# Performance work log

Measured on AMD Instinct MI355X. Metric: run time of the kernel, lower is better.

The kernel has to match this reference:

```python
import jax, jax.numpy as jnp
import numpy as np

N = 50000      # nodes
E = 800000     # edges (avg degree 16)
D = 128        # d_model
C = 2          # num_classes
F_IN = 8       # GCNConv(8, d_model)


def setup_inputs() -> dict:
    key = jax.random.key(0)
    ks = jax.random.split(key, 12)
    s = 0.05  # weight init scale
    return {
        "feature_vec": jax.random.normal(ks[0], (N, F_IN), dtype=jnp.float32),
        "bboxes": jax.random.uniform(ks[1], (N, 4), dtype=jnp.float32),
        "bbox_indices": jnp.arange(N, dtype=jnp.int64) if jax.config.jax_enable_x64 else jnp.arange(N, dtype=jnp.int32),
        "edge_index": jax.random.randint(ks[2], (2, E), 0, N, dtype=jnp.int32),
        "W1": jax.random.normal(ks[3], (F_IN, D), dtype=jnp.float32) * s,
        "b1": jnp.zeros((D,), dtype=jnp.float32),
        "W2": jax.random.normal(ks[4], (D, D), dtype=jnp.float32) * s,
        "b2": jnp.zeros((D,), dtype=jnp.float32),
        "lin1_W": jax.random.normal(ks[5], (2 * D, D), dtype=jnp.float32) * s,
        "lin1_b": jnp.zeros((D,), dtype=jnp.float32),
        "linf_W": jax.random.normal(ks[6], (D, C), dtype=jnp.float32) * s,
        "linf_b": jnp.zeros((C,), dtype=jnp.float32),
    }


def gcn_conv(x, W, b, edge_index, n):
    """PyG GCNConv: add self-loops, symmetric D^-1/2 A D^-1/2 normalization."""
    x = x @ W                                   # [n, out]
    sl = jnp.arange(n, dtype=edge_index.dtype)
    row = jnp.concatenate([edge_index[0], sl])  # source
    col = jnp.concatenate([edge_index[1], sl])  # target
    ones = jnp.ones(row.shape[0], dtype=x.dtype)
    deg = jax.ops.segment_sum(ones, col, num_segments=n)  # >= 1 due to self-loops
    dinv = jax.lax.rsqrt(deg)
    norm = dinv[row] * dinv[col]                # [E + n]
    msg = x[row] * norm[:, None]                # gather + scale
    out = jax.ops.segment_sum(msg, col, num_segments=n)   # scatter-aggregate
    return out + b


def reference(feature_vec, bboxes, bbox_indices, edge_index,
              W1, b1, W2, b2, lin1_W, lin1_b, linf_W, linf_b):
    n = feature_vec.shape[0]
    x = jax.nn.relu(gcn_conv(feature_vec, W1, b1, edge_index, n))
    x = jax.nn.relu(gcn_conv(x, W2, b2, edge_index, n))
    x1 = x[edge_index[0]]                        # [E, D]
    x2 = x[edge_index[1]]                        # [E, D]
    xpair = jnp.concatenate([x1, x2], axis=-1)   # [E, 2D]
    xpair = jax.nn.relu(xpair @ lin1_W + lin1_b)
    xfin = xpair @ linf_W + linf_b               # [E, C]
    probs = jax.nn.log_softmax(xfin, axis=-1)
    bbox_pairs = jnp.concatenate([bboxes[edge_index[0]], bboxes[edge_index[1]]], axis=-1)  # [E, 8]
    bbox_index_pairs = jnp.stack([bbox_indices[edge_index[0]], bbox_indices[edge_index[1]]], axis=1)  # [E, 2]
    return (probs, bbox_pairs, bbox_index_pairs)
```

## Files before the change

kernel.cpp:

```cpp
#include <hip/hip_runtime.h>
#include <hip/hip_bf16.h>
#include <math.h>


typedef __attribute__((ext_vector_type(8))) short short8;
typedef __attribute__((ext_vector_type(4))) float f32x4;
typedef __attribute__((ext_vector_type(2))) float fv2;

__device__ inline ushort f2bf(float f) {
    union { __hip_bfloat16 h; ushort u; } cv;
    cv.h = __float2bfloat16(f);
    return cv.u;
}
__device__ inline float bf2f(ushort u) {
    union { float f; uint u; } c;
    c.u = ((uint)u) << 16;
    return c.f;
}
__device__ inline uchar f2fp8(float f) {
    uint p = __builtin_amdgcn_cvt_pk_fp8_f32(f, f, 0u, false);
    return (uchar)(p & 0xffu);
}

__global__ void k_hist(const int* __restrict__ col, int* __restrict__ cnt, int E) {
    int e = blockIdx.x * blockDim.x + threadIdx.x;
    if (e < E) atomicAdd(&cnt[col[e]], 1);
}

__global__ __launch_bounds__(1024) void k_bsum(const int* __restrict__ cnt,
                                               int* __restrict__ bsum, int N) {
    __shared__ int ts[1024];
    const int b = blockIdx.x, t = threadIdx.x;
    const int i0 = b * 2048 + 2 * t;
    int a0 = (i0 < N) ? cnt[i0] : 0;
    int a1 = (i0 + 1 < N) ? cnt[i0 + 1] : 0;
    ts[t] = a0 + a1;
    __syncthreads();
#pragma unroll
    for (int off = 512; off > 0; off >>= 1) {
        if (t < off) ts[t] += ts[t + off];
        __syncthreads();
    }
    if (t == 0) bsum[b] = ts[0];
}

__global__ __launch_bounds__(1024) void k_scanw(const int* __restrict__ cnt,
                                                const int* __restrict__ bsum,
                                                int* __restrict__ ptr, int N, int E) {
    __shared__ int ts[1024];
    const int b = blockIdx.x, t = threadIdx.x;
    int boff = 0;
    for (int i = 0; i < b; ++i) boff += bsum[i];
    const int i0 = b * 2048 + 2 * t;
    const int a0 = (i0 < N) ? cnt[i0] : 0;
    const int a1 = (i0 + 1 < N) ? cnt[i0 + 1] : 0;
    const int s = a0 + a1;
    ts[t] = s;
    __syncthreads();
    for (int off = 1; off < 1024; off <<= 1) {
        int v = (t >= off) ? ts[t - off] : 0;
        __syncthreads();
        ts[t] += v;
        __syncthreads();
    }
    const int excl = boff + ts[t] - s;
    if (i0 < N) ptr[i0] = excl;
    if (i0 + 1 < N) ptr[i0 + 1] = excl + a0;
    if (b == 0 && t == 0) ptr[N] = E;
}

__global__ void k_fill(const int* __restrict__ row, const int* __restrict__ col,
                       const int* __restrict__ cnt, const int* __restrict__ ptr,
                       int* __restrict__ cursor, int2* __restrict__ eadj, int E) {
    int e = blockIdx.x * blockDim.x + threadIdx.x;
    if (e >= E) return;
    int r = row[e], c = col[e];
    float dr = rsqrtf(1.0f + (float)cnt[r]);
    float dc = rsqrtf(1.0f + (float)cnt[c]);
    int p = ptr[c] + atomicAdd(&cursor[c], 1);
    eadj[p] = make_int2(r, __float_as_int(dr * dc));
}

__global__ void k_prepWuv(const float* __restrict__ W, ushort* __restrict__ Wuv) {
    int tid = blockIdx.x * blockDim.x + threadIdx.x;
    if (tid >= 256 * 128) return;
    int c = tid >> 7, k = tid & 127;
    int krow = k + ((c >> 7) << 7);
    Wuv[tid] = f2bf(W[krow * 128 + (c & 127)]);
}
__global__ void k_prepW2(const float* __restrict__ W, ushort* __restrict__ Wt) {
    int tid = blockIdx.x * blockDim.x + threadIdx.x;
    if (tid >= 128 * 128) return;
    int n = tid >> 7, k = tid & 127;
    Wt[tid] = f2bf(W[k * 128 + n]);
}

__global__ __launch_bounds__(256) void k_agg8(const float* __restrict__ feat,
                                              const int* __restrict__ cnt,
                                              const int* __restrict__ ptr,
                                              const int2* __restrict__ eadj,
                                              float* __restrict__ aggF, int N) {
    int lane8 = threadIdx.x & 7;
    int node = blockIdx.x * 32 + (threadIdx.x >> 3);
    if (node >= N) return;
    float dd = 1.0f / (1.0f + (float)cnt[node]);
    float acc = feat[(size_t)node * 8 + lane8] * dd;
    int i = ptr[node], end = ptr[node + 1];
    for (; i < end; ++i) {
        const int2 a = eadj[i];
        acc += feat[(size_t)a.x * 8 + lane8] * __int_as_float(a.y);
    }
    aggF[(size_t)node * 8 + lane8] = acc;
}

__global__ __launch_bounds__(256) void k_gemm1(const float* __restrict__ aggF,
                                               const float* __restrict__ W1,
                                               const float* __restrict__ b1,
                                               ushort* __restrict__ x1, int total) {
    int tid = blockIdx.x * blockDim.x + threadIdx.x;
    if (tid >= total) return;
    int n = tid >> 7, j = tid & 127;
    float acc = b1[j];
#pragma unroll
    for (int k = 0; k < 8; ++k) acc += aggF[(size_t)n * 8 + k] * W1[k * 128 + j];
    x1[tid] = f2bf(fmaxf(acc, 0.f));
}

__global__ __launch_bounds__(256) void k_gemm2(const ushort* __restrict__ x1,
                                               const ushort* __restrict__ W2t,
                                               ushort* __restrict__ h2, int N) {
    __shared__ ushort ldsW[128 * 128];
    const int tid = threadIdx.x;
    const int wave = tid >> 6, lane = tid & 63;
    const int m = lane & 15, kb = lane >> 4;
    const int n0 = blockIdx.x * 64;

    const int node_a = min(n0 + wave * 16 + m, N - 1);
    short8 a[4];
#pragma unroll
    for (int kk = 0; kk < 4; ++kk) {
        a[kk] = *reinterpret_cast<const short8*>(&x1[(size_t)node_a * 128 + kk * 32 + kb * 8]);
    }

    {
        char* lb = reinterpret_cast<char*>(ldsW);
        const short8* wg = reinterpret_cast<const short8*>(W2t);
#pragma unroll
        for (int i = 0; i < 8; ++i) {
            const int g = i * 256 + tid;
            const int bo = g * 16;
            const int swz = bo ^ (((bo >> 8) & 7) << 4);
            *reinterpret_cast<short8*>(lb + swz) = wg[g];
        }
    }
    __syncthreads();

    f32x4 acc[8];
#pragma unroll
    for (int t = 0; t < 8; ++t) acc[t] = (f32x4){0.f, 0.f, 0.f, 0.f};

    const char* lbr = reinterpret_cast<const char*>(ldsW);
    const int mswz = (m & 7) << 4;
#pragma unroll
    for (int kk = 0; kk < 4; ++kk) {
#pragma unroll
        for (int t = 0; t < 8; ++t) {
            const int bo = (t * 16 + m) * 256 + kk * 64 + kb * 16;
            const short8 b = *reinterpret_cast<const short8*>(lbr + (bo ^ mswz));
            acc[t] = __builtin_amdgcn_mfma_f32_16x16x32_bf16(a[kk], b, acc[t], 0, 0, 0);
        }
    }

#pragma unroll
    for (int r = 0; r < 4; ++r) {
        const int node = n0 + wave * 16 + kb * 4 + r;
        if (node < N) {
#pragma unroll
            for (int t = 0; t < 8; ++t) {
                h2[(size_t)node * 128 + t * 16 + m] = f2bf(acc[t][r]);
            }
        }
    }
}

__global__ __launch_bounds__(256) void k_gather2(const ushort* __restrict__ h2,
                                                 const int* __restrict__ cnt,
                                                 const int* __restrict__ ptr,
                                                 const int2* __restrict__ eadj,
                                                 const float* __restrict__ b2,
                                                 ushort* __restrict__ xbf, int N) {
    int lane16 = threadIdx.x & 15;
    int node = blockIdx.x * 16 + (threadIdx.x >> 4);
    if (node >= N) return;
    float dd = 1.0f / (1.0f + (float)cnt[node]);
    float acc[8];
    {
        const short8 v = *reinterpret_cast<const short8*>(&h2[(size_t)node * 128 + lane16 * 8]);
#pragma unroll
        for (int i = 0; i < 8; ++i) acc[i] = bf2f((ushort)v[i]) * dd;
    }
    int i = ptr[node], end = ptr[node + 1];
    for (; i < end; ++i) {
        const int2 aa = eadj[i];
        const int s = aa.x;
        const float nm = __int_as_float(aa.y);
        const short8 v = *reinterpret_cast<const short8*>(&h2[(size_t)s * 128 + lane16 * 8]);
#pragma unroll
        for (int q = 0; q < 8; ++q) acc[q] += bf2f((ushort)v[q]) * nm;
    }
    short8 r;
#pragma unroll
    for (int q = 0; q < 8; ++q) {
        r[q] = (short)f2bf(fmaxf(acc[q] + b2[lane16 * 8 + q], 0.f));
    }
    *reinterpret_cast<short8*>(&xbf[(size_t)node * 128 + lane16 * 8]) = r;
}

__global__ __launch_bounds__(512) void k_gemm_uv(const ushort* __restrict__ xbf,
                                                 const ushort* __restrict__ Wuv,
                                                 const float* __restrict__ lin1b,
                                                 uchar* __restrict__ uv, int N) {
    __shared__ ushort ldsW[256 * 128];
    const int tid = threadIdx.x;
    const int wave = tid >> 6, lane = tid & 63;
    const int m = lane & 15, kb = lane >> 4;
    const int ng = wave >> 1;
    const int ch = wave & 1;
    const int n0 = blockIdx.x * 64 + ng * 16;

    const int node_a = min(n0 + m, N - 1);
    short8 a[4];
#pragma unroll
    for (int kk = 0; kk < 4; ++kk) {
        a[kk] = *reinterpret_cast<const short8*>(&xbf[(size_t)node_a * 128 + kk * 32 + kb * 8]);
    }

    {
        char* lb = reinterpret_cast<char*>(ldsW);
        const short8* wg = reinterpret_cast<const short8*>(Wuv);
#pragma unroll
        for (int i = 0; i < 8; ++i) {
            const int g = i * 512 + tid;
            const int bo = g * 16;
            const int swz = bo ^ (((bo >> 8) & 7) << 4);
            *reinterpret_cast<short8*>(lb + swz) = wg[g];
        }
    }
    __syncthreads();

    f32x4 acc[8];
#pragma unroll
    for (int t = 0; t < 8; ++t) acc[t] = (f32x4){0.f, 0.f, 0.f, 0.f};

    const char* lbr = reinterpret_cast<const char*>(ldsW);
    const int mswz = (m & 7) << 4;
#pragma unroll
    for (int kk = 0; kk < 4; ++kk) {
#pragma unroll
        for (int t = 0; t < 8; ++t) {
            const int bo = (ch * 128 + t * 16 + m) * 256 + kk * 64 + kb * 16;
            const short8 b = *reinterpret_cast<const short8*>(lbr + (bo ^ mswz));
            acc[t] = __builtin_amdgcn_mfma_f32_16x16x32_bf16(a[kk], b, acc[t], 0, 0, 0);
        }
    }

#pragma unroll
    for (int r = 0; r < 4; ++r) {
        const int node = n0 + kb * 4 + r;
        if (node < N) {
#pragma unroll
            for (int t = 0; t < 8; ++t) {
                const int c = t * 16 + m;
                float av = acc[t][r];
                if (ch == 0) av += lin1b[c];
                uv[(size_t)node * 256 + ch * 128 + c] = f2fp8(av);
            }
        }
    }
}

__global__ __launch_bounds__(256) void k_edge_lite(const uchar* __restrict__ uv,
                                                   const float* __restrict__ linfW,
                                                   const float* __restrict__ linfb,
                                                   const float* __restrict__ bboxes,
                                                   const int* __restrict__ bidx,
                                                   const int* __restrict__ row,
                                                   const int* __restrict__ col,
                                                   float* __restrict__ out_probs,
                                                   float* __restrict__ out_bbox,
                                                   float* __restrict__ out_bidx,
                                                   int E) {
    const int lane16 = threadIdx.x & 15;
    const int slot = threadIdx.x >> 4;
    float wd[8];
#pragma unroll
    for (int j = 0; j < 8; ++j) {
        const int c = lane16 * 8 + j;
        wd[j] = linfW[c * 2] - linfW[c * 2 + 1];
    }
    const float bias_d = linfb[0] - linfb[1];
    const int step = gridDim.x * 16;
    for (int e = blockIdx.x * 16 + slot; e < E; e += step) {
        const int s = row[e], d = col[e];
        const uint2 ua = *reinterpret_cast<const uint2*>(&uv[(size_t)s * 256 + lane16 * 8]);
        const uint2 va = *reinterpret_cast<const uint2*>(&uv[(size_t)d * 256 + 128 + lane16 * 8]);
        const fv2 u01 = __builtin_amdgcn_cvt_pk_f32_fp8(ua.x, false);
        const fv2 u23 = __builtin_amdgcn_cvt_pk_f32_fp8(ua.x, true);
        const fv2 u45 = __builtin_amdgcn_cvt_pk_f32_fp8(ua.y, false);
        const fv2 u67 = __builtin_amdgcn_cvt_pk_f32_fp8(ua.y, true);
        const fv2 v01 = __builtin_amdgcn_cvt_pk_f32_fp8(va.x, false);
        const fv2 v23 = __builtin_amdgcn_cvt_pk_f32_fp8(va.x, true);
        const fv2 v45 = __builtin_amdgcn_cvt_pk_f32_fp8(va.y, false);
        const fv2 v67 = __builtin_amdgcn_cvt_pk_f32_fp8(va.y, true);
        float p;
        {
            float h0 = fmaxf(u01[0] + v01[0], 0.f);
            float h1 = fmaxf(u01[1] + v01[1], 0.f);
            float h2 = fmaxf(u23[0] + v23[0], 0.f);
            float h3 = fmaxf(u23[1] + v23[1], 0.f);
            float h4 = fmaxf(u45[0] + v45[0], 0.f);
            float h5 = fmaxf(u45[1] + v45[1], 0.f);
            float h6 = fmaxf(u67[0] + v67[0], 0.f);
            float h7 = fmaxf(u67[1] + v67[1], 0.f);
            p = h0 * wd[0];
            p = fmaf(h1, wd[1], p);
            p = fmaf(h2, wd[2], p);
            p = fmaf(h3, wd[3], p);
            p = fmaf(h4, wd[4], p);
            p = fmaf(h5, wd[5], p);
            p = fmaf(h6, wd[6], p);
            p = fmaf(h7, wd[7], p);
        }
#pragma unroll
        for (int t = 1; t < 16; t <<= 1) p += __shfl_xor(p, t);
        if (lane16 < 8) {
            const int node = (lane16 < 4) ? s : d;
            out_bbox[(size_t)e * 8 + lane16] = bboxes[(size_t)node * 4 + (lane16 & 3)];
        } else if (lane16 < 10) {
            const int node = (lane16 == 8) ? s : d;
            out_bidx[(size_t)e * 2 + (lane16 - 8)] = (float)bidx[node];
        } else if (lane16 == 10) {
            const float dd = p + bias_d;
            const float ad = fabsf(dd);
            const float t = -log1pf(expf(-ad));
            const float2 pr = (dd >= 0.f) ? make_float2(t, t - ad) : make_float2(t - ad, t);
            *reinterpret_cast<float2*>(&out_probs[(size_t)e * 2]) = pr;
        }
    }
}

extern "C" void kernel_launch(void* const* d_in, const int* in_sizes, int n_in,
                              void* d_out, int out_size, void* d_ws, size_t ws_size,
                              hipStream_t stream) {
    const float* feat   = (const float*)d_in[0];
    const float* bboxes = (const float*)d_in[1];
    const int*   bidx   = (const int*)d_in[2];
    const int*   eidx   = (const int*)d_in[3];
    const float* W1     = (const float*)d_in[4];
    const float* b1     = (const float*)d_in[5];
    const float* W2     = (const float*)d_in[6];
    const float* b2     = (const float*)d_in[7];
    const float* lin1W  = (const float*)d_in[8];
    const float* lin1b  = (const float*)d_in[9];
    const float* linfW  = (const float*)d_in[10];
    const float* linfb  = (const float*)d_in[11];

    const int N = in_sizes[0] / 8;
    const int E = in_sizes[3] / 2;
    const int* row = eidx;
    const int* col = eidx + E;

    size_t Np = ((size_t)N + 255) & ~255ull;
    size_t Ep = ((size_t)E + 255) & ~255ull;
    size_t A8 = (((size_t)N * 8) + 255) & ~255ull;
    int*    cnt    = (int*)d_ws;
    int*    cursor = cnt + Np;
    int*    ptr    = cursor + Np;
    int*    bsum   = ptr + Np + 256;
    int2*   eadj   = (int2*)(bsum + 256);
    float*  aggF   = (float*)(eadj + Ep);
    ushort* x1     = (ushort*)(aggF + A8);
    ushort* h2     = x1 + (size_t)N * 128;
    uchar*  uvbuf  = (uchar*)(h2 + (size_t)N * 128);
    ushort* Wuv    = (ushort*)(uvbuf + (size_t)N * 256);
    ushort* W2t    = Wuv + 256 * 128;
    ushort* xbf    = x1;

    float* out       = (float*)d_out;
    float* out_probs = out;
    float* out_bbox  = out + (size_t)E * 2;
    float* out_bidx  = out + (size_t)E * 10;

    const int total = N * 128;
    const int B = 256;
    const int nchunk = (N + 2047) / 2048;

    hipMemsetAsync(cnt, 0, 2 * Np * sizeof(int), stream);
    k_hist<<<(E + B - 1) / B, B, 0, stream>>>(col, cnt, E);
    k_bsum<<<nchunk, 1024, 0, stream>>>(cnt, bsum, N);
    k_scanw<<<nchunk, 1024, 0, stream>>>(cnt, bsum, ptr, N, E);
    k_fill<<<(E + B - 1) / B, B, 0, stream>>>(row, col, cnt, ptr, cursor, eadj, E);
    k_prepWuv<<<(256 * 128 + B - 1) / B, B, 0, stream>>>(lin1W, Wuv);
    k_prepW2<<<(128 * 128 + B - 1) / B, B, 0, stream>>>(W2, W2t);

    k_agg8<<<(N + 31) / 32, B, 0, stream>>>(feat, cnt, ptr, eadj, aggF, N);
    k_gemm1<<<(total + B - 1) / B, B, 0, stream>>>(aggF, W1, b1, x1, total);

    k_gemm2<<<(N + 63) / 64, B, 0, stream>>>(x1, W2t, h2, N);
    k_gather2<<<(N + 15) / 16, B, 0, stream>>>(h2, cnt, ptr, eadj, b2, xbf, N);

    k_gemm_uv<<<(N + 63) / 64, 512, 0, stream>>>(xbf, Wuv, lin1b, uvbuf, N);

    k_edge_lite<<<2048, B, 0, stream>>>(uvbuf, linfW, linfb,
                                        bboxes, bidx, row, col,
                                        out_probs, out_bbox, out_bidx, E);
}
```

Before: 261.2 us.

## Use 8 lanes per edge with 16-byte loads and prefetch next edge

The edge kernel now assigns 8 lanes per edge instead of 16. Each lane does 16-byte fp8 loads of the per-node projections, and the reduction needs one fewer shuffle step. The grid-stride loop software-pipelines by loading the next edge's indices and uv rows before computing the current one, to hide gather latency. Output writes are reorganised so bbox, index and prob stores use all 8 lanes. The cost is more registers per thread for the prefetched data and weights.

```diff
diff --git a/kernel.cpp b/kernel.cpp
--- a/kernel.cpp
+++ b/kernel.cpp
@@ -290,62 +290,70 @@
                                                    float* __restrict__ out_bbox,
                                                    float* __restrict__ out_bidx,
                                                    int E) {
-    const int lane16 = threadIdx.x & 15;
-    const int slot = threadIdx.x >> 4;
-    float wd[8];
-#pragma unroll
-    for (int j = 0; j < 8; ++j) {
-        const int c = lane16 * 8 + j;
+    const int lane8 = threadIdx.x & 7;
+    const int slot = threadIdx.x >> 3;
+    int e = blockIdx.x * 32 + slot;
+    if (e >= E) return;
+
+    float wd[16];
+#pragma unroll
+    for (int j = 0; j < 16; ++j) {
+        const int c = lane8 * 16 + j;
         wd[j] = linfW[c * 2] - linfW[c * 2 + 1];
     }
     const float bias_d = linfb[0] - linfb[1];
-    const int step = gridDim.x * 16;
-    for (int e = blockIdx.x * 16 + slot; e < E; e += step) {
-        const int s = row[e], d = col[e];
-        const uint2 ua = *reinterpret_cast<const uint2*>(&uv[(size_t)s * 256 + lane16 * 8]);
-        const uint2 va = *reinterpret_cast<const uint2*>(&uv[(size_t)d * 256 + 128 + lane16 * 8]);
-        const fv2 u01 = __builtin_amdgcn_cvt_pk_f32_fp8(ua.x, false);
-        const fv2 u23 = __builtin_amdgcn_cvt_pk_f32_fp8(ua.x, true);
-        const fv2 u45 = __builtin_amdgcn_cvt_pk_f32_fp8(ua.y, false);
-        const fv2 u67 = __builtin_amdgcn_cvt_pk_f32_fp8(ua.y, true);
-        const fv2 v01 = __builtin_amdgcn_cvt_pk_f32_fp8(va.x, false);
-        const fv2 v23 = __builtin_amdgcn_cvt_pk_f32_fp8(va.x, true);
-        const fv2 v45 = __builtin_amdgcn_cvt_pk_f32_fp8(va.y, false);
-        const fv2 v67 = __builtin_amdgcn_cvt_pk_f32_fp8(va.y, true);
-        float p;
+    const int step = gridDim.x * 32;
+
+    int s = row[e], d = col[e];
+    uint4 ua = *reinterpret_cast<const uint4*>(&uv[(size_t)s * 256 + lane8 * 16]);
+    uint4 va = *reinterpret_cast<const uint4*>(&uv[(size_t)d * 256 + 128 + lane8 * 16]);
+
+    while (true) {
+        const int e2 = e + step;
+        const bool more = (e2 < E);
+        int s2 = 0, d2 = 0;
+        uint4 ua2 = ua, va2 = va;
+        if (more) {
+            s2 = row[e2];
+            d2 = col[e2];
+            ua2 = *reinterpret_cast<const uint4*>(&uv[(size_t)s2 * 256 + lane8 * 16]);
+            va2 = *reinterpret_cast<const uint4*>(&uv[(size_t)d2 * 256 + 128 + lane8 * 16]);
+        }
+
+        float p = 0.f;
         {
-            float h0 = fmaxf(u01[0] + v01[0], 0.f);
-            float h1 = fmaxf(u01[1] + v01[1], 0.f);
-            float h2 = fmaxf(u23[0] + v23[0], 0.f);
-            float h3 = fmaxf(u23[1] + v23[1], 0.f);
-            float h4 = fmaxf(u45[0] + v45[0], 0.f);
-            float h5 = fmaxf(u45[1] + v45[1], 0.f);
-            float h6 = fmaxf(u67[0] + v67[0], 0.f);
-            float h7 = fmaxf(u67[1] + v67[1], 0.f);
-            p = h0 * wd[0];
-            p = fmaf(h1, wd[1], p);
-            p = fmaf(h2, wd[2], p);
-            p = fmaf(h3, wd[3], p);
-            p = fmaf(h4, wd[4], p);
-            p = fmaf(h5, wd[5], p);
-            p = fmaf(h6, wd[6], p);
-            p = fmaf(h7, wd[7], p);
-        }
-#pragma unroll
-        for (int t = 1; t < 16; t <<= 1) p += __shfl_xor(p, t);
-        if (lane16 < 8) {
-            const int node = (lane16 < 4) ? s : d;
-            out_bbox[(size_t)e * 8 + lane16] = bboxes[(size_t)node * 4 + (lane16 & 3)];
-        } else if (lane16 < 10) {
-            const int node = (lane16 == 8) ? s : d;
-            out_bidx[(size_t)e * 2 + (lane16 - 8)] = (float)bidx[node];
-        } else if (lane16 == 10) {
+            const uint uw[4] = {ua.x, ua.y, ua.z, ua.w};
+            const uint vw[4] = {va.x, va.y, va.z, va.w};
+#pragma unroll
+            for (int w = 0; w < 4; ++w) {
+                const fv2 ul = __builtin_amdgcn_cvt_pk_f32_fp8(uw[w], false);
+                const fv2 uh = __builtin_amdgcn_cvt_pk_f32_fp8(uw[w], true);
+                const fv2 vl = __builtin_amdgcn_cvt_pk_f32_fp8(vw[w], false);
+                const fv2 vh = __builtin_amdgcn_cvt_pk_f32_fp8(vw[w], true);
+                p = fmaf(fmaxf(ul[0] + vl[0], 0.f), wd[4 * w + 0], p);
+                p = fmaf(fmaxf(ul[1] + vl[1], 0.f), wd[4 * w + 1], p);
+                p = fmaf(fmaxf(uh[0] + vh[0], 0.f), wd[4 * w + 2], p);
+                p = fmaf(fmaxf(uh[1] + vh[1], 0.f), wd[4 * w + 3], p);
+            }
+        }
+        p += __shfl_xor(p, 1);
+        p += __shfl_xor(p, 2);
+        p += __shfl_xor(p, 4);
+
+        out_bbox[(size_t)e * 8 + lane8] = bboxes[(size_t)((lane8 < 4) ? s : d) * 4 + (lane8 & 3)];
+        if (lane8 == 0) {
+            *reinterpret_cast<float2*>(&out_bidx[(size_t)e * 2]) =
+                make_float2((float)bidx[s], (float)bidx[d]);
+        } else if (lane8 == 1) {
             const float dd = p + bias_d;
             const float ad = fabsf(dd);
             const float t = -log1pf(expf(-ad));
             const float2 pr = (dd >= 0.f) ? make_float2(t, t - ad) : make_float2(t - ad, t);
             *reinterpret_cast<float2*>(&out_probs[(size_t)e * 2]) = pr;
         }
+
+        if (!more) break;
+        e = e2; s = s2; d = d2; ua = ua2; va = va2;
     }
 }
 
```

Measured after the change: 248.1 us. 5.0% less time.
